# Performance work log

Hardware: AMD Instinct MI355X
Metric: run time of the kernel (lower is better)

Reference implementation:

```python
import jax, jax.numpy as jnp
import numpy as np

EPS = 1e-8  # torch F.cosine_similarity default eps


def setup_inputs() -> dict:
    key = jax.random.key(0)
    k1, k2, k3, k4 = jax.random.split(key, 4)
    D, V, C = 512, 512, 2048
    query_key = jax.random.normal(k1, (D,), dtype=jnp.float32)
    W_k = jax.random.normal(k2, (D, D), dtype=jnp.float32) * (1.0 / np.sqrt(D))
    b_k = jnp.zeros((D,), dtype=jnp.float32)
    assoc_matrix = jax.random.normal(k3, (C, D, V), dtype=jnp.float32) * 0.02
    usage_counter = jax.random.uniform(k4, (C,), dtype=jnp.float32) * 10.0
    return {
        "query_key": query_key,
        "W_k": W_k,
        "b_k": b_k,
        "assoc_matrix": assoc_matrix,
        "usage_counter": usage_counter,
        "top_k": 32,
    }


def reference(query_key, W_k, b_k, assoc_matrix, usage_counter, top_k):
    # key_encoder: Linear (x @ W^T + b) followed by tanh
    q = jnp.tanh(query_key @ W_k.T + b_k)  # [D]
    # stored keys = first value-column of each association matrix, as in source
    stored_keys = assoc_matrix[:, :, 0]  # [C, D]
    # batched cosine similarity (replaces python loop of tiny per-slot ops)
    dots = stored_keys @ q  # [C]
    q_norm = jnp.maximum(jnp.sqrt(jnp.sum(q * q)), EPS)
    k_norms = jnp.maximum(jnp.sqrt(jnp.sum(stored_keys * stored_keys, axis=1)), EPS)
    sims = dots / (q_norm * k_norms)  # [C]
    top_sims, top_idx = jax.lax.top_k(sims, top_k)  # [k], [k]
    # confidence = sim * (1 + log(1 + usage))
    confidences = top_sims * (1.0 + jnp.log1p(usage_counter[top_idx]))  # [k]
    # gather-matmul retrieval: q @ A[idx] for each top index
    gathered = assoc_matrix[top_idx]  # [k, D, V]
    retrieved_values = jnp.einsum("d,kdv->kv", q, gathered)  # [k, V]
    return retrieved_values, confidences, top_sims
```

## Files before the change

kernel.cpp:

```cpp
#include <hip/hip_runtime.h>
#include <math.h>

#define DD 512
#define VV 512
#define CC 2048
#define TOPK 32
#define EPSF 1e-8f


__global__ void k1_q(const float* __restrict__ qk, const float* __restrict__ Wk,
                     const float* __restrict__ bk, float* __restrict__ q) {
    int wave = threadIdx.x >> 6;
    int lane = threadIdx.x & 63;
    int row = blockIdx.x * 4 + wave;
    const float4* wrow = (const float4*)(Wk + (size_t)row * DD);
    const float4* qv = (const float4*)qk;
    float4 a0 = wrow[lane], b0 = qv[lane];
    float4 a1 = wrow[lane + 64], b1 = qv[lane + 64];
    float s = a0.x * b0.x + a0.y * b0.y + a0.z * b0.z + a0.w * b0.w
            + a1.x * b1.x + a1.y * b1.y + a1.z * b1.z + a1.w * b1.w;
    #pragma unroll
    for (int off = 32; off; off >>= 1) s += __shfl_down(s, off);
    if (lane == 0) q[row] = tanhf(s + bk[row]);
}

__global__ void k2_sims(const float* __restrict__ assoc, const float* __restrict__ q,
                        float* __restrict__ sims) {
    __shared__ float qs[DD];
    __shared__ float red[4][3];
    int t = threadIdx.x;
    int wv = t >> 6, lane = t & 63;
    qs[t] = q[t];
    qs[t + 256] = q[t + 256];
    __syncthreads();
    int c = blockIdx.x * 2 + (wv >> 1);
    int h = wv & 1;
    const float* base = assoc + (size_t)c * ((size_t)DD * VV) + (size_t)(h * 256) * VV;
    float d = 0.f, n = 0.f, nq = 0.f;
    #pragma unroll
    for (int j = 0; j < 4; ++j) {
        int dd = lane + 64 * j;
        float a = __builtin_nontemporal_load(base + (size_t)dd * VV);
        float qq = qs[h * 256 + dd];
        d += a * qq;
        n += a * a;
        nq += qq * qq;
    }
    #pragma unroll
    for (int off = 32; off; off >>= 1) {
        d += __shfl_down(d, off);
        n += __shfl_down(n, off);
        nq += __shfl_down(nq, off);
    }
    if (lane == 0) { red[wv][0] = d; red[wv][1] = n; red[wv][2] = nq; }
    __syncthreads();
    if (t < 2) {
        float dt  = red[2 * t][0] + red[2 * t + 1][0];
        float nt_ = red[2 * t][1] + red[2 * t + 1][1];
        float nqt = red[2 * t][2] + red[2 * t + 1][2];
        sims[blockIdx.x * 2 + t] =
            dt / (fmaxf(sqrtf(nqt), EPSF) * fmaxf(sqrtf(nt_), EPSF));
    }
}

__global__ void k3_topk(const float* __restrict__ sims_g, const float* __restrict__ usage,
                        int* __restrict__ top_idx, float* __restrict__ out) {
    __shared__ float sims[CC];
    __shared__ int pr[256];
    int t = threadIdx.x;
    for (int i = t; i < CC; i += 256) sims[i] = sims_g[i];
    __syncthreads();
    int lane = t & 63, seg = t >> 6;
    int c = blockIdx.x * 64 + lane;
    float mv = sims[c];
    int rank = 0;
    const float4* s4 = (const float4*)sims;
    int base4 = seg * 128;
    #pragma unroll 8
    for (int i = 0; i < 128; ++i) {
        float4 v = s4[base4 + i];
        int cp = (base4 + i) * 4;
        rank += (v.x > mv) || (v.x == mv && cp     < c);
        rank += (v.y > mv) || (v.y == mv && cp + 1 < c);
        rank += (v.z > mv) || (v.z == mv && cp + 2 < c);
        rank += (v.w > mv) || (v.w == mv && cp + 3 < c);
    }
    pr[t] = rank;
    __syncthreads();
    if (seg == 0) {
        int total = pr[lane] + pr[lane + 64] + pr[lane + 128] + pr[lane + 192];
        if (total < TOPK) {
            top_idx[total] = c;
            out[16384 + total] = mv * (1.0f + log1pf(usage[c]));
            out[16416 + total] = mv;
        }
    }
}

__global__ void k4_direct(const float* __restrict__ assoc, const float* __restrict__ qv,
                          const int* __restrict__ top_idx, float* __restrict__ out) {
    __shared__ float qs[DD];
    __shared__ float red[256];
    int t = threadIdx.x;
    int kk = blockIdx.x >> 3, chunk = blockIdx.x & 7;
    int wv = t >> 6, lane = t & 63;
    int idx = top_idx[kk];
    qs[t] = qv[t];
    qs[t + 256] = qv[t + 256];
    __syncthreads();
    const float* base = assoc + (size_t)idx * ((size_t)DD * VV) + chunk * 64 + lane;
    int r0 = wv * 128;
    float s = 0.f;
    #pragma unroll
    for (int g = 0; g < 2; ++g) {
        float v[64];
        #pragma unroll
        for (int r = 0; r < 64; ++r)
            v[r] = __builtin_nontemporal_load(base + (size_t)(r0 + g * 64 + r) * VV);
        #pragma unroll
        for (int r = 0; r < 64; ++r)
            s += qs[r0 + g * 64 + r] * v[r];
    }
    red[t] = s;
    __syncthreads();
    if (t < 64)
        out[kk * 512 + chunk * 64 + t] = red[t] + red[64 + t] + red[128 + t] + red[192 + t];
}

extern "C" void kernel_launch(void* const* d_in, const int* in_sizes, int n_in,
                              void* d_out, int out_size, void* d_ws, size_t ws_size,
                              hipStream_t stream) {
    const float* qk    = (const float*)d_in[0];
    const float* Wk    = (const float*)d_in[1];
    const float* bk    = (const float*)d_in[2];
    const float* assoc = (const float*)d_in[3];
    const float* usage = (const float*)d_in[4];

    float* ws      = (float*)d_ws;
    float* sims    = ws;
    float* q       = ws + 2048;
    int*   top_idx = (int*)(ws + 2560);
    float* out     = (float*)d_out;

    k1_q     <<<128,  256, 0, stream>>>(qk, Wk, bk, q);
    k2_sims  <<<1024, 256, 0, stream>>>(assoc, q, sims);
    k3_topk  <<<32,   256, 0, stream>>>(sims, usage, top_idx, out);
    k4_direct<<<TOPK * 8, 256, 0, stream>>>(assoc, q, top_idx, out);
}
```

Measured before the change: 50.32 us.

## Fuse top-k selection into similarity kernel via atomic last-blocks counter

Merges the top-k ranking kernel into the similarity kernel. Every block increments a global atomic counter, and the last 32 blocks to finish spin until all 1024 blocks are done, then each ranks one 64-candidate slice from the sims buffer. The counter is reset in the query kernel. This removes one kernel launch and its inter-kernel gap, but the fused kernel carries more shared memory and the tail blocks busy-wait, which could hurt occupancy or deadlock if the late blocks are not all resident.

```diff
diff --git a/kernel.cpp b/kernel.cpp
--- a/kernel.cpp
+++ b/kernel.cpp
@@ -6,10 +6,13 @@
 #define CC 2048
 #define TOPK 32
 #define EPSF 1e-8f
+#define NBLK 1024
 
 
 __global__ void k1_q(const float* __restrict__ qk, const float* __restrict__ Wk,
-                     const float* __restrict__ bk, float* __restrict__ q) {
+                     const float* __restrict__ bk, float* __restrict__ q,
+                     unsigned int* __restrict__ counter) {
+    if (blockIdx.x == 0 && threadIdx.x == 0) counter[0] = 0u;
     int wave = threadIdx.x >> 6;
     int lane = threadIdx.x & 63;
     int row = blockIdx.x * 4 + wave;
@@ -24,10 +27,16 @@
     if (lane == 0) q[row] = tanhf(s + bk[row]);
 }
 
-__global__ void k2_sims(const float* __restrict__ assoc, const float* __restrict__ q,
-                        float* __restrict__ sims) {
+__global__ __launch_bounds__(256) void k2_sims_topk(
+        const float* __restrict__ assoc, const float* __restrict__ q,
+        const float* __restrict__ usage, float* __restrict__ sims,
+        int* __restrict__ top_idx, float* __restrict__ out,
+        unsigned int* __restrict__ counter) {
     __shared__ float qs[DD];
     __shared__ float red[4][3];
+    __shared__ unsigned int oldv;
+    __shared__ float ssims[CC];
+    __shared__ int pr[256];
     int t = threadIdx.x;
     int wv = t >> 6, lane = t & 63;
     qs[t] = q[t];
@@ -60,38 +69,47 @@
         float nqt = red[2 * t][2] + red[2 * t + 1][2];
         sims[blockIdx.x * 2 + t] =
             dt / (fmaxf(sqrtf(nqt), EPSF) * fmaxf(sqrtf(nt_), EPSF));
+        __threadfence();
     }
-}
+    __syncthreads();
+    if (t == 0)
+        oldv = __hip_atomic_fetch_add(counter, 1u, __ATOMIC_ACQ_REL,
+                                      __HIP_MEMORY_SCOPE_AGENT);
+    __syncthreads();
+    unsigned int old = oldv;
+    if (old < (unsigned int)(NBLK - 32)) return;
 
-__global__ void k3_topk(const float* __restrict__ sims_g, const float* __restrict__ usage,
-                        int* __restrict__ top_idx, float* __restrict__ out) {
-    __shared__ float sims[CC];
-    __shared__ int pr[256];
-    int t = threadIdx.x;
-    for (int i = t; i < CC; i += 256) sims[i] = sims_g[i];
+    int slice = (int)old - (NBLK - 32);
+    if (t == 0) {
+        while (__hip_atomic_load(counter, __ATOMIC_ACQUIRE,
+                                 __HIP_MEMORY_SCOPE_AGENT) < (unsigned int)NBLK) {}
+    }
     __syncthreads();
-    int lane = t & 63, seg = t >> 6;
-    int c = blockIdx.x * 64 + lane;
-    float mv = sims[c];
+    __threadfence();
+    for (int i = t; i < CC; i += 256) ssims[i] = sims[i];
+    __syncthreads();
+    int seg = wv;
+    int cc = slice * 64 + lane;
+    float mv = ssims[cc];
     int rank = 0;
-    const float4* s4 = (const float4*)sims;
+    const float4* s4 = (const float4*)ssims;
     int base4 = seg * 128;
     #pragma unroll 8
     for (int i = 0; i < 128; ++i) {
         float4 v = s4[base4 + i];
         int cp = (base4 + i) * 4;
-        rank += (v.x > mv) || (v.x == mv && cp     < c);
-        rank += (v.y > mv) || (v.y == mv && cp + 1 < c);
-        rank += (v.z > mv) || (v.z == mv && cp + 2 < c);
-        rank += (v.w > mv) || (v.w == mv && cp + 3 < c);
+        rank += (v.x > mv) || (v.x == mv && cp     < cc);
+        rank += (v.y > mv) || (v.y == mv && cp + 1 < cc);
+        rank += (v.z > mv) || (v.z == mv && cp + 2 < cc);
+        rank += (v.w > mv) || (v.w == mv && cp + 3 < cc);
     }
     pr[t] = rank;
     __syncthreads();
     if (seg == 0) {
         int total = pr[lane] + pr[lane + 64] + pr[lane + 128] + pr[lane + 192];
         if (total < TOPK) {
-            top_idx[total] = c;
-            out[16384 + total] = mv * (1.0f + log1pf(usage[c]));
+            top_idx[total] = cc;
+            out[16384 + total] = mv * (1.0f + log1pf(usage[cc]));
             out[16416 + total] = mv;
         }
     }
@@ -136,14 +154,14 @@
     const float* assoc = (const float*)d_in[3];
     const float* usage = (const float*)d_in[4];
 
-    float* ws      = (float*)d_ws;
-    float* sims    = ws;
-    float* q       = ws + 2048;
-    int*   top_idx = (int*)(ws + 2560);
-    float* out     = (float*)d_out;
+    float* ws           = (float*)d_ws;
+    float* sims         = ws;
+    float* q            = ws + 2048;
+    int*   top_idx      = (int*)(ws + 2560);
+    unsigned int* cnt   = (unsigned int*)(ws + 2592);
+    float* out          = (float*)d_out;
 
-    k1_q     <<<128,  256, 0, stream>>>(qk, Wk, bk, q);
-    k2_sims  <<<1024, 256, 0, stream>>>(assoc, q, sims);
-    k3_topk  <<<32,   256, 0, stream>>>(sims, usage, top_idx, out);
-    k4_direct<<<TOPK * 8, 256, 0, stream>>>(assoc, q, top_idx, out);
+    k1_q        <<<128,  256, 0, stream>>>(qk, Wk, bk, q, cnt);
+    k2_sims_topk<<<NBLK, 256, 0, stream>>>(assoc, q, usage, sims, top_idx, out, cnt);
+    k4_direct   <<<TOPK * 8, 256, 0, stream>>>(assoc, q, top_idx, out);
 }
```

Measured after the change: 119.7 us. 2.38x slower.
